# Performance work log

Hardware: AMD Instinct MI355X
Metric: run time of the kernel (lower is better)

The kernel has to match this reference:

```python
import jax, jax.numpy as jnp
import numpy as np
from jax import lax

D_MODEL, D_INNER, D_CONV, DT_RANK, D_STATE, SEQ_LEN = 1024, 2048, 4, 64, 16, 4096


def setup_inputs() -> dict:
    key = jax.random.key(0)
    ks = jax.random.split(key, 9)
    s = 0.02
    x = jax.random.normal(ks[0], (SEQ_LEN, D_MODEL), dtype=jnp.float32)
    W_in = jax.random.normal(ks[1], (2 * D_INNER, D_MODEL), dtype=jnp.float32) * s
    conv_w = jax.random.normal(ks[2], (D_INNER, 1, D_CONV), dtype=jnp.float32) * 0.2  # depthwise (O,I/g,K)
    conv_b = jax.random.normal(ks[3], (D_INNER,), dtype=jnp.float32) * s
    W_x = jax.random.normal(ks[4], (DT_RANK + 2 * D_STATE, D_INNER), dtype=jnp.float32) * s
    W_dt = jax.random.normal(ks[5], (D_INNER, DT_RANK), dtype=jnp.float32) * s
    b_dt = jax.random.normal(ks[6], (D_INNER,), dtype=jnp.float32) * s
    # canonical S4D-real init: A[d, n] = n+1 -> A_log = log(1..d_state), tiled over d_inner
    A_log = jnp.log(jnp.tile(jnp.arange(1, D_STATE + 1, dtype=jnp.float32), (D_INNER, 1)))
    D = jnp.ones((D_INNER,), dtype=jnp.float32)
    W_out = jax.random.normal(ks[7], (D_MODEL, D_INNER), dtype=jnp.float32) * s
    return {"x": x, "W_in": W_in, "conv_w": conv_w, "conv_b": conv_b,
            "W_x": W_x, "W_dt": W_dt, "b_dt": b_dt, "A_log": A_log, "D": D,
            "W_out": W_out}


def _causal_depthwise_conv(x_ld, conv_w, conv_b):
    # x_ld: (L, d_inner). eqx Conv1d with padding=d_conv-1 then [:, :L] == left-pad causal conv.
    k = conv_w.shape[-1]
    xp = jnp.pad(x_ld, ((k - 1, 0), (0, 0)))  # (L+k-1, d)
    lhs = xp.T[None]  # (1, d, L+k-1)
    out = lax.conv_general_dilated(
        lhs, conv_w, window_strides=(1,), padding='VALID',
        dimension_numbers=('NCH', 'OIH', 'NCH'),
        feature_group_count=x_ld.shape[1])  # (1, d, L)
    return (out[0] + conv_b[:, None]).T  # (L, d)


def reference(x, W_in, conv_w, conv_b, W_x, W_dt, b_dt, A_log, D, W_out):
    L = x.shape[0]
    d_inner, d_state = A_log.shape
    dt_rank = W_dt.shape[1]

    xr = x @ W_in.T                      # (L, 2*d_inner)
    xi, res = jnp.split(xr, 2, axis=-1)  # each (L, d_inner)
    xs = jax.nn.silu(_causal_depthwise_conv(xi, conv_w, conv_b))  # (L, d_inner)

    # selective SSM
    dbl = xs @ W_x.T                     # (L, dt_rank + 2*d_state)
    dt_in, B, C = jnp.split(dbl, [dt_rank, dt_rank + d_state], axis=-1)
    delta = jax.nn.softplus(dt_in @ W_dt.T + b_dt)       # (L, d_inner)
    A = -jnp.exp(A_log)                                  # (d_inner, d_state)
    dA = jnp.exp(delta[:, :, None] * A[None])            # (L, d, n)
    dBu = delta[:, :, None] * B[:, None, :] * xs[:, :, None]  # (L, d, n)

    def step(h, ab):
        a, b = ab
        h = a * h + b
        return h, h

    _, hs = lax.scan(step, jnp.zeros((d_inner, d_state), dtype=x.dtype), (dA, dBu))
    y = jnp.einsum('ldn,ln->ld', hs, C) + xs * D         # (L, d_inner)

    y = y * jax.nn.silu(res)
    return y @ W_out.T                                   # (L, d_model)
```

## Files before the change

kernel.cpp:

```cpp
#include <hip/hip_runtime.h>
#include <cstdint>
#include <cstddef>

#define LSEQ 4096
#define DM 1024
#define DI 2048
#define DCONV 4
#define DRNK 64
#define DSTATE 16
#define DXW 96
#define NCH 64
#define CLEN 64
#define KSPLIT 8

typedef unsigned short ushort_t;
typedef __bf16 bfx8 __attribute__((ext_vector_type(8)));
typedef float  fx4  __attribute__((ext_vector_type(4)));
typedef float  fx16 __attribute__((ext_vector_type(16)));
typedef ushort_t usx8 __attribute__((ext_vector_type(8)));

__device__ __forceinline__ float siluf(float x) { return x / (1.f + __expf(-x)); }
__device__ __forceinline__ float softplusf(float x) {
  return fmaxf(x, 0.f) + log1pf(__expf(-fabsf(x)));
}
__device__ __forceinline__ ushort_t f2b(float x) {
  __bf16 b = (__bf16)x;
  return __builtin_bit_cast(ushort_t, b);
}
__device__ __forceinline__ float b2f(ushort_t u) {
  unsigned int x = ((unsigned int)u) << 16;
  return __builtin_bit_cast(float, x);
}
__device__ __forceinline__ void async16(const void* g, void* l) {
  __builtin_amdgcn_global_load_lds(
      (const __attribute__((address_space(1))) unsigned int*)g,
      (__attribute__((address_space(3))) unsigned int*)l, 16, 0, 0);
}

template <int EPI, int BN>
__global__ __launch_bounds__(256) void gemm32(
    const ushort_t* __restrict__ A, int lda,
    const ushort_t* __restrict__ B, int ldb,
    void* __restrict__ Cv, int ldc, int K)
{
  constexpr int MI = 2;
  constexpr int NJ = BN / 64;
  __shared__ ushort_t As[128 * 64];
  __shared__ ushort_t Bs[BN * 64];
  const int tid  = threadIdx.x;
  const int m0   = blockIdx.y * 128, n0 = blockIdx.x * BN;
  const int lane = tid & 63;
  const int wave = tid >> 6;
  const int wm   = (wave >> 1) * 64, wn = (wave & 1) * (BN / 2);
  const int lm   = lane & 31;
  const int kg   = lane >> 5;
  const int r0  = tid >> 3;
  const int pos = tid & 7;
  const int cswz = (pos ^ (r0 & 7)) * 8;
  const int key  = lm & 7;

  fx16 acc[MI][NJ] = {};

  const ushort_t* ga = A + (size_t)(m0 + r0) * lda + cswz;
  const ushort_t* gb = B + (size_t)(n0 + r0) * ldb + cswz;

  for (int k0 = 0; k0 < K; k0 += 64) {
#pragma unroll
    for (int t = 0; t < 4; ++t)
      async16(ga + (size_t)(32 * t) * lda + k0, &As[t * 32 * 64 + tid * 8]);
#pragma unroll
    for (int t = 0; t < BN / 32; ++t)
      async16(gb + (size_t)(32 * t) * ldb + k0, &Bs[t * 32 * 64 + tid * 8]);
    __syncthreads();

#pragma unroll
    for (int kk = 0; kk < 4; ++kk) {
      const int swz = ((kk * 2 + kg) ^ key) * 8;
      bfx8 af[MI], bfr[NJ];
#pragma unroll
      for (int i = 0; i < MI; ++i)
        af[i] = *(const bfx8*)&As[(wm + i * 32 + lm) * 64 + swz];
#pragma unroll
      for (int j = 0; j < NJ; ++j)
        bfr[j] = *(const bfx8*)&Bs[(wn + j * 32 + lm) * 64 + swz];
#pragma unroll
      for (int i = 0; i < MI; ++i)
#pragma unroll
        for (int j = 0; j < NJ; ++j)
          acc[i][j] = __builtin_amdgcn_mfma_f32_32x32x16_bf16(af[i], bfr[j], acc[i][j], 0, 0, 0);
    }
    __syncthreads();
  }

#pragma unroll
  for (int i = 0; i < MI; ++i)
#pragma unroll
    for (int j = 0; j < NJ; ++j)
#pragma unroll
      for (int r = 0; r < 16; ++r) {
        const int lrow = (r & 3) + 8 * (r >> 2) + 4 * kg;
        const size_t rowoff =
            (size_t)(m0 + wm + i * 32 + lrow) * ldc + n0 + wn + j * 32 + lm;
        if (EPI == 1) ((ushort_t*)Cv)[rowoff] = f2b(acc[i][j][r]);
        else          ((float*)Cv)[rowoff]   = acc[i][j][r];
      }
}

__global__ __launch_bounds__(256) void gemm_delta(
    const ushort_t* __restrict__ A,
    const ushort_t* __restrict__ B,
    const float* __restrict__ bias,
    ushort_t* __restrict__ C)
{
  __shared__ ushort_t As[128 * 64];
  __shared__ ushort_t Bs[128 * 64];
  const int tid  = threadIdx.x;
  const int m0   = blockIdx.y * 128, n0 = blockIdx.x * 128;
  const int lane = tid & 63;
  const int wave = tid >> 6;
  const int wm   = (wave >> 1) * 64, wn = (wave & 1) * 64;
  const int lm   = lane & 31;
  const int kg   = lane >> 5;
  const int r0  = tid >> 3;
  const int pos = tid & 7;
  const int cswz = (pos ^ (r0 & 7)) * 8;
  const int key  = lm & 7;

  fx16 acc[2][2] = {};

#pragma unroll
  for (int t = 0; t < 4; ++t)
    async16(A + (size_t)(m0 + r0 + 32 * t) * DRNK + cswz, &As[t * 32 * 64 + tid * 8]);
#pragma unroll
  for (int t = 0; t < 4; ++t)
    async16(B + (size_t)(n0 + r0 + 32 * t) * DRNK + cswz, &Bs[t * 32 * 64 + tid * 8]);
  __syncthreads();

#pragma unroll
  for (int kk = 0; kk < 4; ++kk) {
    const int swz = ((kk * 2 + kg) ^ key) * 8;
    bfx8 af[2], bfr[2];
#pragma unroll
    for (int i = 0; i < 2; ++i)
      af[i] = *(const bfx8*)&As[(wm + i * 32 + lm) * 64 + swz];
#pragma unroll
    for (int j = 0; j < 2; ++j)
      bfr[j] = *(const bfx8*)&Bs[(wn + j * 32 + lm) * 64 + swz];
#pragma unroll
    for (int i = 0; i < 2; ++i)
#pragma unroll
      for (int j = 0; j < 2; ++j)
        acc[i][j] = __builtin_amdgcn_mfma_f32_32x32x16_bf16(af[i], bfr[j], acc[i][j], 0, 0, 0);
  }

#pragma unroll
  for (int i = 0; i < 2; ++i)
#pragma unroll
    for (int j = 0; j < 2; ++j) {
      const int col = n0 + wn + j * 32 + lm;
      const float bv = bias[col];
#pragma unroll
      for (int r = 0; r < 16; ++r) {
        const int lrow = (r & 3) + 8 * (r >> 2) + 4 * kg;
        C[(size_t)(m0 + wm + i * 32 + lrow) * DI + col] =
            f2b(softplusf(acc[i][j][r] + bv));
      }
    }
}

__global__ __launch_bounds__(256) void gemm_dbl(
    const ushort_t* __restrict__ A, const ushort_t* __restrict__ B,
    float* __restrict__ P)
{
  __shared__ ushort_t As[128 * 32];
  __shared__ ushort_t Bs[128 * 32];
  const int tid  = threadIdx.x;
  const int m0   = blockIdx.y * 128;
  const int lane = tid & 63;
  const int wave = tid >> 6;
  const int wm   = (wave >> 1) * 64, wn = (wave & 1) * 48;
  const int lm   = lane & 15;
  const int r0 = tid >> 2;
  const int cswz = (((tid & 3) ^ ((r0 >> 1) & 3))) * 8;
  const int swz  = (((lane >> 4) ^ ((lm >> 1) & 3))) * 8;
  const int kbeg = blockIdx.z * (DI / KSPLIT);

  fx4 acc[4][3] = {};

  const int brow1 = (r0 + 64 < DXW) ? r0 + 64 : DXW - 1;
  const ushort_t* ga  = A + (size_t)(m0 + r0) * DI + kbeg + cswz;
  const ushort_t* gb0 = B + (size_t)r0 * DI + kbeg + cswz;
  const ushort_t* gb1 = B + (size_t)brow1 * DI + kbeg + cswz;
  ushort_t* la0 = &As[r0 * 32 + (tid & 3) * 8];
  ushort_t* la1 = &As[(r0 + 64) * 32 + (tid & 3) * 8];
  ushort_t* lb0 = &Bs[r0 * 32 + (tid & 3) * 8];
  ushort_t* lb1 = &Bs[(r0 + 64) * 32 + (tid & 3) * 8];

  for (int k0 = 0; k0 < DI / KSPLIT; k0 += 32) {
    async16(ga + k0, la0);
    async16(ga + (size_t)64 * DI + k0, la1);
    async16(gb0 + k0, lb0);
    async16(gb1 + k0, lb1);
    __syncthreads();

    bfx8 af[4], bfr[3];
#pragma unroll
    for (int i = 0; i < 4; ++i)
      af[i] = *(const bfx8*)&As[(wm + i * 16 + lm) * 32 + swz];
#pragma unroll
    for (int j = 0; j < 3; ++j)
      bfr[j] = *(const bfx8*)&Bs[(wn + j * 16 + lm) * 32 + swz];
#pragma unroll
    for (int i = 0; i < 4; ++i)
#pragma unroll
      for (int j = 0; j < 3; ++j)
        acc[i][j] = __builtin_amdgcn_mfma_f32_16x16x32_bf16(af[i], bfr[j], acc[i][j], 0, 0, 0);
    __syncthreads();
  }

  float* base = P + (size_t)blockIdx.z * LSEQ * DXW;
  const int crow = (lane >> 4) * 4;
  const int ccol = lane & 15;
#pragma unroll
  for (int i = 0; i < 4; ++i)
#pragma unroll
    for (int r = 0; r < 4; ++r) {
      float* cp = base + (size_t)(m0 + wm + i * 16 + crow + r) * DXW + wn + ccol;
#pragma unroll
      for (int j = 0; j < 3; ++j)
        cp[j * 16] = acc[i][j][r];
    }
}

__global__ __launch_bounds__(256) void reduce_dbl(
    const float* __restrict__ P, ushort_t* __restrict__ dtb,
    float* __restrict__ dblBC)
{
  const int f = blockIdx.x * 256 + threadIdx.x;
  float s = 0.f;
#pragma unroll
  for (int z = 0; z < KSPLIT; ++z) s += P[(size_t)z * LSEQ * DXW + f];
  const int l = f / DXW;
  const int c = f - l * DXW;
  if (c < DRNK) dtb[(size_t)l * DRNK + c] = f2b(s);
  else          dblBC[(size_t)l * 32 + (c - DRNK)] = s;
}

#define CSZ0 (LSEQ * DM)
#define CSZ1 (2 * DI * DM)
#define CSZ2 (DM * DI)
#define CSZ3 (DXW * DI)
#define CSZ4 (DI * DRNK)
#define CTOT (CSZ0 + CSZ1 + CSZ2 + CSZ3 + CSZ4)

__global__ __launch_bounds__(256) void cast_all(
    const float* __restrict__ x, const float* __restrict__ W_in,
    const float* __restrict__ W_out, const float* __restrict__ W_x,
    const float* __restrict__ W_dt,
    ushort_t* __restrict__ xb, ushort_t* __restrict__ W_inb,
    ushort_t* __restrict__ W_outb, ushort_t* __restrict__ W_xb,
    ushort_t* __restrict__ W_dtb)
{
  int i = (blockIdx.x * 256 + threadIdx.x) * 4;
  if (i >= CTOT) return;
  const float* src; ushort_t* dst;
  if (i < CSZ0) { src = x + i; dst = xb + i; }
  else if (i < CSZ0 + CSZ1) { int o = i - CSZ0; src = W_in + o; dst = W_inb + o; }
  else if (i < CSZ0 + CSZ1 + CSZ2) { int o = i - CSZ0 - CSZ1; src = W_out + o; dst = W_outb + o; }
  else if (i < CSZ0 + CSZ1 + CSZ2 + CSZ3) { int o = i - CSZ0 - CSZ1 - CSZ2; src = W_x + o; dst = W_xb + o; }
  else { int o = i - CSZ0 - CSZ1 - CSZ2 - CSZ3; src = W_dt + o; dst = W_dtb + o; }
  float4 v = *(const float4*)src;
  ushort4 o4;
  o4.x = f2b(v.x); o4.y = f2b(v.y); o4.z = f2b(v.z); o4.w = f2b(v.w);
  *(ushort4*)dst = o4;
}

__global__ __launch_bounds__(256) void conv2(
    const ushort_t* __restrict__ xrb, const float* __restrict__ cw,
    const float* __restrict__ cb, ushort_t* __restrict__ xsb)
{
  const int d0 = threadIdx.x * 8;
  const int l0 = blockIdx.x * 8;

  float4 w[8];
#pragma unroll
  for (int j = 0; j < 8; ++j) w[j] = *(const float4*)(cw + (size_t)(d0 + j) * DCONV);
  float cbv[8];
  *(float4*)&cbv[0] = *(const float4*)(cb + d0);
  *(float4*)&cbv[4] = *(const float4*)(cb + d0 + 4);

  float h0[8], h1[8], h2[8];
#pragma unroll
  for (int j = 0; j < 8; ++j) { h0[j] = 0.f; h1[j] = 0.f; h2[j] = 0.f; }
  if (l0 >= 3) {
    usx8 u0 = *(const usx8*)(xrb + (size_t)(l0 - 3) * (2 * DI) + d0);
    usx8 u1 = *(const usx8*)(xrb + (size_t)(l0 - 2) * (2 * DI) + d0);
    usx8 u2 = *(const usx8*)(xrb + (size_t)(l0 - 1) * (2 * DI) + d0);
#pragma unroll
    for (int j = 0; j < 8; ++j) { h0[j] = b2f(u0[j]); h1[j] = b2f(u1[j]); h2[j] = b2f(u2[j]); }
  }

#pragma unroll
  for (int i = 0; i < 8; ++i) {
    const int l = l0 + i;
    usx8 uc = *(const usx8*)(xrb + (size_t)l * (2 * DI) + d0);
    float c[8];
#pragma unroll
    for (int j = 0; j < 8; ++j) c[j] = b2f(uc[j]);
    usx8 o;
#pragma unroll
    for (int j = 0; j < 8; ++j) {
      float acc = cbv[j];
      acc = fmaf(w[j].x, h0[j], acc);
      acc = fmaf(w[j].y, h1[j], acc);
      acc = fmaf(w[j].z, h2[j], acc);
      acc = fmaf(w[j].w, c[j], acc);
      o[j] = f2b(siluf(acc));
    }
    *(usx8*)(xsb + (size_t)l * DI + d0) = o;
#pragma unroll
    for (int j = 0; j < 8; ++j) { h0[j] = h1[j]; h1[j] = h2[j]; h2[j] = c[j]; }
  }
}

__device__ __forceinline__ bool chain_ok(const float* Av) {
  bool ok = true;
#pragma unroll
  for (int n = 0; n < DSTATE; ++n)
    ok = ok && (fabsf(Av[n] + (float)(n + 1)) < 1e-4f);
  return ok;
}

__global__ __launch_bounds__(256) void scan_pass1(
    const ushort_t* __restrict__ deltab, const ushort_t* __restrict__ xsb,
    const float* __restrict__ dblBC, const float* __restrict__ A_log,
    float* __restrict__ sd, float* __restrict__ cS)
{
  const int tid = threadIdx.x;
  const int g = blockIdx.x;
  const int c = blockIdx.y;
  const int d = g * 256 + tid;
  __shared__ ushort_t Dsh[CLEN * 256];
  __shared__ ushort_t Ush[CLEN * 256];
  __shared__ float Bsh[CLEN][DSTATE];

  const size_t rowbase = (size_t)(c * CLEN) * DI + g * 256;
  for (int i = tid; i < CLEN * 32; i += 256) {
    const int l = i >> 5;
    const int o = (i & 31) * 8;
    *(usx8*)&Dsh[l * 256 + o] = *(const usx8*)(deltab + rowbase + (size_t)l * DI + o);
    *(usx8*)&Ush[l * 256 + o] = *(const usx8*)(xsb   + rowbase + (size_t)l * DI + o);
  }
  for (int i = tid; i < CLEN * DSTATE; i += 256) {
    const int l = i >> 4, n = i & 15;
    Bsh[l][n] = dblBC[(size_t)(c * CLEN + l) * 32 + n];
  }
  __syncthreads();

  float Av[DSTATE], h[DSTATE];
#pragma unroll
  for (int n = 0; n < DSTATE; ++n) {
    Av[n] = -__expf(A_log[d * DSTATE + n]);
    h[n] = 0.f;
  }
  const size_t base = (size_t)c * DI * DSTATE + (size_t)d * DSTATE;
  float sdv = 0.f;

  if (chain_ok(Av)) {
    for (int l = 0; l < CLEN; ++l) {
      const float dlt = b2f(Dsh[l * 256 + tid]);
      const float du = dlt * b2f(Ush[l * 256 + tid]);
      sdv += dlt;
      const float q = __expf(-dlt);
      float dAn = 1.f;
#pragma unroll
      for (int n = 0; n < DSTATE; ++n) {
        dAn *= q;
        h[n] = fmaf(dAn, h[n], du * Bsh[l][n]);
      }
    }
  } else {
    for (int l = 0; l < CLEN; ++l) {
      const float dlt = b2f(Dsh[l * 256 + tid]);
      const float du = dlt * b2f(Ush[l * 256 + tid]);
      sdv += dlt;
#pragma unroll
      for (int n = 0; n < DSTATE; ++n) {
        const float dA = __expf(dlt * Av[n]);
        h[n] = fmaf(dA, h[n], du * Bsh[l][n]);
      }
    }
  }
  sd[(size_t)c * DI + d] = sdv;
#pragma unroll
  for (int n = 0; n < DSTATE; ++n) cS[base + n] = h[n];
}

__global__ __launch_bounds__(64) void scan_pass2(
    const float* __restrict__ sd, const float* __restrict__ cS,
    const float* __restrict__ A_log, float* __restrict__ ch0)
{
  const int dn = blockIdx.x * 64 + threadIdx.x;
  const int d = dn >> 4;
  const float av = -__expf(A_log[dn]);
  float h = 0.f;
  for (int c = 0; c < NCH; ++c) {
    const size_t o = (size_t)c * DI * DSTATE + dn;
    const float s = cS[o];
    const float p = __expf(av * sd[(size_t)c * DI + d]);
    ch0[o] = h;
    h = fmaf(p, h, s);
  }
}

__global__ __launch_bounds__(256) void scan_pass3(
    const ushort_t* __restrict__ deltab, const ushort_t* __restrict__ xsb,
    const float* __restrict__ dblBC, const float* __restrict__ A_log,
    const float* __restrict__ ch0, const float* __restrict__ Dp,
    const ushort_t* __restrict__ xrb, ushort_t* __restrict__ y1b)
{
  const int tid = threadIdx.x;
  const int g = blockIdx.x;
  const int c = blockIdx.y;
  const int d = g * 256 + tid;
  __shared__ ushort_t Dsh[CLEN * 256];
  __shared__ ushort_t Ush[CLEN * 256];
  __shared__ float Bsh[CLEN][DSTATE];
  __shared__ float Csh[CLEN][DSTATE];

  const size_t rowbase = (size_t)(c * CLEN) * DI + g * 256;
  for (int i = tid; i < CLEN * 32; i += 256) {
    const int l = i >> 5;
    const int o = (i & 31) * 8;
    *(usx8*)&Dsh[l * 256 + o] = *(const usx8*)(deltab + rowbase + (size_t)l * DI + o);
    *(usx8*)&Ush[l * 256 + o] = *(const usx8*)(xsb   + rowbase + (size_t)l * DI + o);
  }
  for (int i = tid; i < CLEN * DSTATE; i += 256) {
    const int l = i >> 4, n = i & 15;
    const size_t row = (size_t)(c * CLEN + l) * 32;
    Bsh[l][n] = dblBC[row + n];
    Csh[l][n] = dblBC[row + 16 + n];
  }
  __syncthreads();

  float Av[DSTATE], h[DSTATE];
  const size_t base = (size_t)c * DI * DSTATE + (size_t)d * DSTATE;
#pragma unroll
  for (int n = 0; n < DSTATE; ++n) {
    Av[n] = -__expf(A_log[d * DSTATE + n]);
    h[n] = ch0[base + n];
  }
  const float Dd = Dp[d];
  const ushort_t* resp = xrb + (size_t)(c * CLEN) * (2 * DI) + DI + d;
  ushort_t* yp = y1b + (size_t)(c * CLEN) * DI + d;

  if (chain_ok(Av)) {
    for (int l = 0; l < CLEN; ++l) {
      const float dlt = b2f(Dsh[l * 256 + tid]);
      const float u = b2f(Ush[l * 256 + tid]);
      const float du = dlt * u;
      const float q = __expf(-dlt);
      float dAn = 1.f;
      float y = 0.f;
#pragma unroll
      for (int n = 0; n < DSTATE; ++n) {
        dAn *= q;
        h[n] = fmaf(dAn, h[n], du * Bsh[l][n]);
        y = fmaf(h[n], Csh[l][n], y);
      }
      y = fmaf(u, Dd, y);
      const float res = b2f(resp[(size_t)l * (2 * DI)]);
      yp[(size_t)l * DI] = f2b(y * siluf(res));
    }
  } else {
    for (int l = 0; l < CLEN; ++l) {
      const float dlt = b2f(Dsh[l * 256 + tid]);
      const float u = b2f(Ush[l * 256 + tid]);
      const float du = dlt * u;
      float y = 0.f;
#pragma unroll
      for (int n = 0; n < DSTATE; ++n) {
        const float dA = __expf(dlt * Av[n]);
        h[n] = fmaf(dA, h[n], du * Bsh[l][n]);
        y = fmaf(h[n], Csh[l][n], y);
      }
      y = fmaf(u, Dd, y);
      const float res = b2f(resp[(size_t)l * (2 * DI)]);
      yp[(size_t)l * DI] = f2b(y * siluf(res));
    }
  }
}

extern "C" void kernel_launch(void* const* d_in, const int* in_sizes, int n_in,
                              void* d_out, int out_size, void* d_ws, size_t ws_size,
                              hipStream_t stream) {
  (void)in_sizes; (void)n_in; (void)out_size; (void)ws_size;
  const float* x      = (const float*)d_in[0];
  const float* W_in   = (const float*)d_in[1];
  const float* conv_w = (const float*)d_in[2];
  const float* conv_b = (const float*)d_in[3];
  const float* W_x    = (const float*)d_in[4];
  const float* W_dt   = (const float*)d_in[5];
  const float* b_dt   = (const float*)d_in[6];
  const float* A_log  = (const float*)d_in[7];
  const float* Dp     = (const float*)d_in[8];
  const float* W_out  = (const float*)d_in[9];
  float* out = (float*)d_out;

  float* ws    = (float*)d_ws;
  float* sd    = ws;
  float* cS    = sd + (size_t)NCH * DI;
  float* ch0   = cS + (size_t)NCH * DI * DSTATE;
  ushort_t* deltab = (ushort_t*)(ch0 + (size_t)NCH * DI * DSTATE);
  ushort_t* xrb   = deltab + (size_t)LSEQ * DI;
  ushort_t* xsb   = xrb   + (size_t)LSEQ * 2 * DI;
  ushort_t* y1b   = xsb   + (size_t)LSEQ * DI;
  ushort_t* xb    = y1b   + (size_t)LSEQ * DI;
  ushort_t* W_inb = xb    + (size_t)LSEQ * DM;
  ushort_t* W_outb= W_inb + (size_t)2 * DI * DM;
  ushort_t* W_xb  = W_outb+ (size_t)DM * DI;
  ushort_t* W_dtb = W_xb  + (size_t)DXW * DI;
  ushort_t* dtb   = W_dtb + (size_t)DI * DRNK;
  float* dblBC = (float*)(dtb + (size_t)LSEQ * DRNK);
  float* partial = ws;

  hipLaunchKernelGGL(cast_all, dim3((CTOT / 4 + 255) / 256), dim3(256), 0, stream,
                     x, W_in, W_out, W_x, W_dt, xb, W_inb, W_outb, W_xb, W_dtb);

  hipLaunchKernelGGL(HIP_KERNEL_NAME(gemm32<1, 128>),
                     dim3((2 * DI) / 128, LSEQ / 128), dim3(256), 0, stream,
                     xb, DM, W_inb, DM, (void*)xrb, 2 * DI, DM);

  hipLaunchKernelGGL(conv2, dim3(LSEQ / 8), dim3(256), 0, stream,
                     xrb, conv_w, conv_b, xsb);

  hipLaunchKernelGGL(gemm_dbl, dim3(1, LSEQ / 128, KSPLIT), dim3(256), 0, stream,
                     xsb, W_xb, partial);
  hipLaunchKernelGGL(reduce_dbl, dim3((LSEQ * DXW) / 256), dim3(256), 0, stream,
                     partial, dtb, dblBC);

  hipLaunchKernelGGL(gemm_delta, dim3(DI / 128, LSEQ / 128), dim3(256), 0, stream,
                     dtb, W_dtb, b_dt, deltab);

  hipLaunchKernelGGL(scan_pass1, dim3(DI / 256, NCH), dim3(256), 0, stream,
                     deltab, xsb, dblBC, A_log, sd, cS);
  hipLaunchKernelGGL(scan_pass2, dim3((DI * DSTATE) / 64), dim3(64), 0, stream,
                     sd, cS, A_log, ch0);
  hipLaunchKernelGGL(scan_pass3, dim3(DI / 256, NCH), dim3(256), 0, stream,
                     deltab, xsb, dblBC, A_log, ch0, Dp, xrb, y1b);

  hipLaunchKernelGGL(HIP_KERNEL_NAME(gemm32<0, 64>),
                     dim3(DM / 64, LSEQ / 128), dim3(256), 0, stream,
                     y1b, DI, W_outb, DI, (void*)out, DM, DI);
}
```

Before: 287.9 us.

## Use 256x128 tiles with 512 threads for in-projection GEMM and retile dbl GEMM

Adds a gemm_wide kernel that computes the in-projection with 256x128 output tiles per 512-thread block, so each B tile is reused across twice as many rows and fewer blocks are launched. The x_dbl split-K GEMM switches from 16x16x32 to 32x32x16 MFMA, loads 64-wide K slices, and drops the clamped duplicate B row loads. The larger block and shared-memory footprint may reduce occupancy, and the coarser grid leaves fewer blocks to fill the CUs.

```diff
diff --git a/kernel.cpp b/kernel.cpp
--- a/kernel.cpp
+++ b/kernel.cpp
@@ -35,6 +35,71 @@
   __builtin_amdgcn_global_load_lds(
       (const __attribute__((address_space(1))) unsigned int*)g,
       (__attribute__((address_space(3))) unsigned int*)l, 16, 0, 0);
+}
+
+__global__ __launch_bounds__(512) void gemm_wide(
+    const ushort_t* __restrict__ A, int lda,
+    const ushort_t* __restrict__ B, int ldb,
+    ushort_t* __restrict__ C, int ldc, int K)
+{
+  __shared__ ushort_t As[256 * 64];
+  __shared__ ushort_t Bs[128 * 64];
+  const int tid  = threadIdx.x;
+  const int m0   = blockIdx.y * 256, n0 = blockIdx.x * 128;
+  const int lane = tid & 63;
+  const int wave = tid >> 6;
+  const int wm   = (wave >> 1) * 64;
+  const int wn   = (wave & 1) * 64;
+  const int lm   = lane & 31;
+  const int kg   = lane >> 5;
+  const int r0  = tid >> 3;
+  const int pos = tid & 7;
+  const int cswz = (pos ^ (r0 & 7)) * 8;
+  const int key  = lm & 7;
+
+  fx16 acc[2][2] = {};
+
+  const ushort_t* ga = A + (size_t)(m0 + r0) * lda + cswz;
+  const ushort_t* gb = B + (size_t)(n0 + r0) * ldb + cswz;
+
+  for (int k0 = 0; k0 < K; k0 += 64) {
+#pragma unroll
+    for (int t = 0; t < 4; ++t)
+      async16(ga + (size_t)(64 * t) * lda + k0, &As[t * 64 * 64 + tid * 8]);
+#pragma unroll
+    for (int t = 0; t < 2; ++t)
+      async16(gb + (size_t)(64 * t) * ldb + k0, &Bs[t * 64 * 64 + tid * 8]);
+    __syncthreads();
+
+#pragma unroll
+    for (int kk = 0; kk < 4; ++kk) {
+      const int swz = ((kk * 2 + kg) ^ key) * 8;
+      bfx8 af[2], bfr[2];
+#pragma unroll
+      for (int i = 0; i < 2; ++i)
+        af[i] = *(const bfx8*)&As[(wm + i * 32 + lm) * 64 + swz];
+#pragma unroll
+      for (int j = 0; j < 2; ++j)
+        bfr[j] = *(const bfx8*)&Bs[(wn + j * 32 + lm) * 64 + swz];
+#pragma unroll
+      for (int i = 0; i < 2; ++i)
+#pragma unroll
+        for (int j = 0; j < 2; ++j)
+          acc[i][j] = __builtin_amdgcn_mfma_f32_32x32x16_bf16(af[i], bfr[j], acc[i][j], 0, 0, 0);
+    }
+    __syncthreads();
+  }
+
+#pragma unroll
+  for (int i = 0; i < 2; ++i)
+#pragma unroll
+    for (int j = 0; j < 2; ++j)
+#pragma unroll
+      for (int r = 0; r < 16; ++r) {
+        const int lrow = (r & 3) + 8 * (r >> 2) + 4 * kg;
+        C[(size_t)(m0 + wm + i * 32 + lrow) * ldc + n0 + wn + j * 32 + lm] =
+            f2b(acc[i][j][r]);
+      }
 }
 
 template <int EPI, int BN>
@@ -172,63 +237,57 @@
     const ushort_t* __restrict__ A, const ushort_t* __restrict__ B,
     float* __restrict__ P)
 {
-  __shared__ ushort_t As[128 * 32];
-  __shared__ ushort_t Bs[128 * 32];
+  __shared__ ushort_t As[128 * 64];
+  __shared__ ushort_t Bs[96 * 64];
   const int tid  = threadIdx.x;
   const int m0   = blockIdx.y * 128;
   const int lane = tid & 63;
   const int wave = tid >> 6;
-  const int wm   = (wave >> 1) * 64, wn = (wave & 1) * 48;
-  const int lm   = lane & 15;
-  const int r0 = tid >> 2;
-  const int cswz = (((tid & 3) ^ ((r0 >> 1) & 3))) * 8;
-  const int swz  = (((lane >> 4) ^ ((lm >> 1) & 3))) * 8;
+  const int wm   = wave * 32;
+  const int lm   = lane & 31;
+  const int kg   = lane >> 5;
+  const int r0  = tid >> 3;
+  const int pos = tid & 7;
+  const int cswz = (pos ^ (r0 & 7)) * 8;
+  const int key  = lm & 7;
   const int kbeg = blockIdx.z * (DI / KSPLIT);
 
-  fx4 acc[4][3] = {};
-
-  const int brow1 = (r0 + 64 < DXW) ? r0 + 64 : DXW - 1;
-  const ushort_t* ga  = A + (size_t)(m0 + r0) * DI + kbeg + cswz;
-  const ushort_t* gb0 = B + (size_t)r0 * DI + kbeg + cswz;
-  const ushort_t* gb1 = B + (size_t)brow1 * DI + kbeg + cswz;
-  ushort_t* la0 = &As[r0 * 32 + (tid & 3) * 8];
-  ushort_t* la1 = &As[(r0 + 64) * 32 + (tid & 3) * 8];
-  ushort_t* lb0 = &Bs[r0 * 32 + (tid & 3) * 8];
-  ushort_t* lb1 = &Bs[(r0 + 64) * 32 + (tid & 3) * 8];
-
-  for (int k0 = 0; k0 < DI / KSPLIT; k0 += 32) {
-    async16(ga + k0, la0);
-    async16(ga + (size_t)64 * DI + k0, la1);
-    async16(gb0 + k0, lb0);
-    async16(gb1 + k0, lb1);
+  fx16 acc[3] = {};
+
+  const ushort_t* ga = A + (size_t)(m0 + r0) * DI + kbeg + cswz;
+  const ushort_t* gb = B + (size_t)r0 * DI + kbeg + cswz;
+
+  for (int k0 = 0; k0 < DI / KSPLIT; k0 += 64) {
+#pragma unroll
+    for (int t = 0; t < 4; ++t)
+      async16(ga + (size_t)(32 * t) * DI + k0, &As[t * 32 * 64 + tid * 8]);
+#pragma unroll
+    for (int t = 0; t < 3; ++t)
+      async16(gb + (size_t)(32 * t) * DI + k0, &Bs[t * 32 * 64 + tid * 8]);
     __syncthreads();
 
-    bfx8 af[4], bfr[3];
-#pragma unroll
-    for (int i = 0; i < 4; ++i)
-      af[i] = *(const bfx8*)&As[(wm + i * 16 + lm) * 32 + swz];
-#pragma unroll
-    for (int j = 0; j < 3; ++j)
-      bfr[j] = *(const bfx8*)&Bs[(wn + j * 16 + lm) * 32 + swz];
-#pragma unroll
-    for (int i = 0; i < 4; ++i)
+#pragma unroll
+    for (int kk = 0; kk < 4; ++kk) {
+      const int swz = ((kk * 2 + kg) ^ key) * 8;
+      bfx8 af = *(const bfx8*)&As[(wm + lm) * 64 + swz];
+      bfx8 bfr[3];
 #pragma unroll
       for (int j = 0; j < 3; ++j)
-        acc[i][j] = __builtin_amdgcn_mfma_f32_16x16x32_bf16(af[i], bfr[j], acc[i][j], 0, 0, 0);
+        bfr[j] = *(const bfx8*)&Bs[(j * 32 + lm) * 64 + swz];
+#pragma unroll
+      for (int j = 0; j < 3; ++j)
+        acc[j] = __builtin_amdgcn_mfma_f32_32x32x16_bf16(af, bfr[j], acc[j], 0, 0, 0);
+    }
     __syncthreads();
   }
 
   float* base = P + (size_t)blockIdx.z * LSEQ * DXW;
-  const int crow = (lane >> 4) * 4;
-  const int ccol = lane & 15;
-#pragma unroll
-  for (int i = 0; i < 4; ++i)
-#pragma unroll
-    for (int r = 0; r < 4; ++r) {
-      float* cp = base + (size_t)(m0 + wm + i * 16 + crow + r) * DXW + wn + ccol;
-#pragma unroll
-      for (int j = 0; j < 3; ++j)
-        cp[j * 16] = acc[i][j][r];
+#pragma unroll
+  for (int j = 0; j < 3; ++j)
+#pragma unroll
+    for (int r = 0; r < 16; ++r) {
+      const int lrow = (r & 3) + 8 * (r >> 2) + 4 * kg;
+      base[(size_t)(m0 + wm + lrow) * DXW + j * 32 + lm] = acc[j][r];
     }
 }
 
@@ -527,9 +586,8 @@
   hipLaunchKernelGGL(cast_all, dim3((CTOT / 4 + 255) / 256), dim3(256), 0, stream,
                      x, W_in, W_out, W_x, W_dt, xb, W_inb, W_outb, W_xb, W_dtb);
 
-  hipLaunchKernelGGL(HIP_KERNEL_NAME(gemm32<1, 128>),
-                     dim3((2 * DI) / 128, LSEQ / 128), dim3(256), 0, stream,
-                     xb, DM, W_inb, DM, (void*)xrb, 2 * DI, DM);
+  hipLaunchKernelGGL(gemm_wide, dim3((2 * DI) / 128, LSEQ / 256), dim3(512), 0, stream,
+                     xb, DM, W_inb, DM, xrb, 2 * DI, DM);
 
   hipLaunchKernelGGL(conv2, dim3(LSEQ / 8), dim3(256), 0, stream,
                      xrb, conv_w, conv_b, xsb);
```

Result: faster. 279.9 us (-2.8%).
